# Performance work log

Hardware: AMD Instinct MI355X
Metric: run time of the kernel (lower is better)

The kernel has to match this reference:

```python
import jax, jax.numpy as jnp
import numpy as np

N_ENT = 50000
N_REL = 500
N_EDGE = 800000
H_DIM = 96
BN_EPS = 1e-5


def setup_inputs() -> dict:
    key = jax.random.key(0)
    k1, k2, k3, k4, k5 = jax.random.split(key, 5)
    return {
        "ent_emb": jax.random.normal(k1, (N_ENT, H_DIM), dtype=jnp.float32),
        "rel_emb": jax.random.normal(k2, (N_REL, H_DIM), dtype=jnp.float32),
        "neigh_w": jax.random.normal(k3, (H_DIM, H_DIM), dtype=jnp.float32) * (1.0 / np.sqrt(H_DIM)),
        "bn_gamma": jnp.ones((H_DIM,), dtype=jnp.float32),
        "bn_beta": jnp.zeros((H_DIM,), dtype=jnp.float32),
        "rel_id": jax.random.randint(k4, (N_EDGE,), 0, N_REL, dtype=jnp.int64),
        "dst": jax.random.randint(k5, (N_EDGE,), 0, N_ENT, dtype=jnp.int64),
    }


def reference(ent_emb, rel_emb, neigh_w, bn_gamma, bn_beta, rel_id, dst):
    n_nodes = ent_emb.shape[0]
    # per-edge gather: edge feature = relation embedding  [E, D]
    e = rel_emb[rel_id]
    # e_dot_v: dot of edge feature with destination node embedding  [E]
    score = jnp.sum(e * ent_emb[dst], axis=-1)
    # edge softmax over incoming edges of each destination node
    seg_max = jax.ops.segment_max(score, dst, num_segments=n_nodes)  # [N]
    w = jnp.exp(score - seg_max[dst])                                # [E]
    seg_sum = jax.ops.segment_sum(w, dst, num_segments=n_nodes)      # [N]
    alpha = w / seg_sum[dst]                                         # [E]
    # weighted scatter-sum aggregation into destination nodes  [N, D]
    neigh = jax.ops.segment_sum(e * alpha[:, None], dst, num_segments=n_nodes)
    # linear
    out = neigh @ neigh_w
    # BatchNorm1d (training mode: batch stats over nodes, biased var)
    mu = jnp.mean(out, axis=0)
    var = jnp.mean((out - mu) ** 2, axis=0)
    out = (out - mu) * jax.lax.rsqrt(var + BN_EPS) * bn_gamma + bn_beta
    return jnp.tanh(out)
```

## Files before the change

kernel.cpp:

```cpp
#include <hip/hip_runtime.h>
#include <math.h>

#define N_ENT   50000
#define N_REL   500
#define N_EDGE  800000
#define H       96
#define BN_EPS  1e-5f
#define DEG_CAP 64

#define RELW_BLOCKS ((N_REL * H + 255) / 256)
#define ZERO_N      (N_ENT + 2 * H)
#define ZERO_BLOCKS ((ZERO_N + 255) / 256)

__global__ __launch_bounds__(256) void k_init(
        const float* __restrict__ rel, const float* __restrict__ W,
        float* __restrict__ relW, unsigned* __restrict__ zbase) {
    if (blockIdx.x < RELW_BLOCKS) {
        __shared__ float Ws[H * H];
        for (int i = threadIdx.x; i < H * H; i += 256) Ws[i] = W[i];
        __syncthreads();
        int t = blockIdx.x * 256 + threadIdx.x;
        if (t >= N_REL * H) return;
        int r = t / H;
        int c = t - r * H;
        const float4* rr = (const float4*)(rel + (size_t)r * H);
        float acc = 0.0f;
#pragma unroll
        for (int i = 0; i < H / 4; ++i) {
            float4 a = rr[i];
            acc += a.x * Ws[(4 * i + 0) * H + c];
            acc += a.y * Ws[(4 * i + 1) * H + c];
            acc += a.z * Ws[(4 * i + 2) * H + c];
            acc += a.w * Ws[(4 * i + 3) * H + c];
        }
        relW[t] = acc;
    } else {
        int i = (blockIdx.x - RELW_BLOCKS) * 256 + threadIdx.x;
        if (i < ZERO_N) zbase[i] = 0u;
    }
}

__global__ __launch_bounds__(256) void k_bucket(
        const int* __restrict__ dst, const int* __restrict__ rel_id,
        int* __restrict__ cursor, unsigned short* __restrict__ pay) {
    int e = blockIdx.x * 256 + threadIdx.x;
    if (e >= N_EDGE) return;
    int d = dst[e];
    int r = rel_id[e];
    int p = atomicAdd(cursor + d, 1);
    if (p < DEG_CAP) pay[d * DEG_CAP + p] = (unsigned short)r;
}

__global__ __launch_bounds__(256) void k_node(
        const float* __restrict__ ent, const float* __restrict__ rel,
        const unsigned short* __restrict__ pay, const int* __restrict__ cursor,
        const float* __restrict__ relW, float* __restrict__ out) {
    __shared__ float sh_w[4][DEG_CAP];
    __shared__ int   sh_r[4][DEG_CAP];
    int wv   = threadIdx.x >> 6;
    int lane = threadIdx.x & 63;
    int n = blockIdx.x * 4 + wv;
    if (n >= N_ENT) return;
    int cnt = min(cursor[n], DEG_CAP);

    {
        int q  = lane & 3;
        int jj = lane >> 2;
        const float4* er = (const float4*)(ent + (size_t)n * H) + q * 6;
        float4 e0 = er[0], e1 = er[1], e2 = er[2], e3 = er[3], e4 = er[4], e5 = er[5];
        int npass = (cnt + 15) >> 4;
        for (int p = 0; p < npass; ++p) {
            int j = (p << 4) + jj;
            bool valid = (j < cnt);
            int rid = valid ? (int)pay[n * DEG_CAP + j] : 0;
            float part = 0.0f;
            if (valid) {
                const float4* rr = (const float4*)(rel + (size_t)rid * H) + q * 6;
                float4 b;
                b = rr[0]; part += e0.x*b.x + e0.y*b.y + e0.z*b.z + e0.w*b.w;
                b = rr[1]; part += e1.x*b.x + e1.y*b.y + e1.z*b.z + e1.w*b.w;
                b = rr[2]; part += e2.x*b.x + e2.y*b.y + e2.z*b.z + e2.w*b.w;
                b = rr[3]; part += e3.x*b.x + e3.y*b.y + e3.z*b.z + e3.w*b.w;
                b = rr[4]; part += e4.x*b.x + e4.y*b.y + e4.z*b.z + e4.w*b.w;
                b = rr[5]; part += e5.x*b.x + e5.y*b.y + e5.z*b.z + e5.w*b.w;
            }
            part += __shfl_xor(part, 1);
            part += __shfl_xor(part, 2);
            if (valid && q == 0) { sh_w[wv][j] = part; sh_r[wv][j] = rid; }
        }
    }

    {
        float sc = (lane < cnt) ? sh_w[wv][lane] : -INFINITY;
        float m = sc;
#pragma unroll
        for (int off = 1; off < 64; off <<= 1)
            m = fmaxf(m, __shfl_xor(m, off));
        float w = (lane < cnt) ? __expf(sc - m) : 0.0f;
        float s = w;
#pragma unroll
        for (int off = 1; off < 64; off <<= 1)
            s += __shfl_xor(s, off);
        float inv = (cnt > 0) ? 1.0f / s : 0.0f;
        if (lane < cnt) sh_w[wv][lane] = w * inv;
    }

    int g  = lane & 7;
    int es = lane >> 3;
    float4 a0 = make_float4(0.f, 0.f, 0.f, 0.f);
    float4 a1 = make_float4(0.f, 0.f, 0.f, 0.f);
    float4 a2 = make_float4(0.f, 0.f, 0.f, 0.f);
    for (int k = es; k < cnt; k += 8) {
        float w  = sh_w[wv][k];
        int rid  = sh_r[wv][k];
        const float4* p = (const float4*)(relW + (size_t)rid * H + g * 12);
        float4 f0 = p[0], f1 = p[1], f2 = p[2];
        a0.x += w * f0.x; a0.y += w * f0.y; a0.z += w * f0.z; a0.w += w * f0.w;
        a1.x += w * f1.x; a1.y += w * f1.y; a1.z += w * f1.z; a1.w += w * f1.w;
        a2.x += w * f2.x; a2.y += w * f2.y; a2.z += w * f2.z; a2.w += w * f2.w;
    }
#pragma unroll
    for (int off = 8; off < 64; off <<= 1) {
        a0.x += __shfl_xor(a0.x, off); a0.y += __shfl_xor(a0.y, off);
        a0.z += __shfl_xor(a0.z, off); a0.w += __shfl_xor(a0.w, off);
        a1.x += __shfl_xor(a1.x, off); a1.y += __shfl_xor(a1.y, off);
        a1.z += __shfl_xor(a1.z, off); a1.w += __shfl_xor(a1.w, off);
        a2.x += __shfl_xor(a2.x, off); a2.y += __shfl_xor(a2.y, off);
        a2.z += __shfl_xor(a2.z, off); a2.w += __shfl_xor(a2.w, off);
    }
    if (es == 0) {
        float4* op = (float4*)(out + (size_t)n * H + g * 12);
        op[0] = a0; op[1] = a1; op[2] = a2;
    }
}

__global__ __launch_bounds__(256) void k_bnstats(
        const float* __restrict__ out, float* __restrict__ bn_sum,
        float* __restrict__ bn_sumsq) {
    __shared__ float sh_s[4][H], sh_q[4][H];
    int wave = threadIdx.x >> 6;
    int lane = threadIdx.x & 63;
    float4 s = make_float4(0.f, 0.f, 0.f, 0.f);
    float4 ss = make_float4(0.f, 0.f, 0.f, 0.f);
    if (lane < H / 4) {
        for (int n = blockIdx.x * 4 + wave; n < N_ENT; n += gridDim.x * 4) {
            float4 v = ((const float4*)(out + (size_t)n * H))[lane];
            s.x += v.x; s.y += v.y; s.z += v.z; s.w += v.w;
            ss.x += v.x * v.x; ss.y += v.y * v.y;
            ss.z += v.z * v.z; ss.w += v.w * v.w;
        }
        ((float4*)sh_s[wave])[lane] = s;
        ((float4*)sh_q[wave])[lane] = ss;
    }
    __syncthreads();
    int d = threadIdx.x;
    if (d < H) {
        float ts = sh_s[0][d] + sh_s[1][d] + sh_s[2][d] + sh_s[3][d];
        float tq = sh_q[0][d] + sh_q[1][d] + sh_q[2][d] + sh_q[3][d];
        atomicAdd(bn_sum + d, ts);
        atomicAdd(bn_sumsq + d, tq);
    }
}

__device__ __forceinline__ float fast_tanh(float x) {
    return 1.0f - 2.0f / (__expf(2.0f * x) + 1.0f);
}

__global__ __launch_bounds__(256) void k_bnapply(
        float* __restrict__ out, const float* __restrict__ bn_sum,
        const float* __restrict__ bn_sumsq, const float* __restrict__ gamma,
        const float* __restrict__ beta) {
    int t = blockIdx.x * 256 + threadIdx.x;
    if (t >= N_ENT * H / 4) return;
    int c4 = t % (H / 4);
    const float inv_n = 1.0f / (float)N_ENT;
    float4 v = ((const float4*)out)[t];
    float4 sm = ((const float4*)bn_sum)[c4];
    float4 sq = ((const float4*)bn_sumsq)[c4];
    float4 g  = ((const float4*)gamma)[c4];
    float4 b  = ((const float4*)beta)[c4];
    float mu0 = sm.x * inv_n, mu1 = sm.y * inv_n, mu2 = sm.z * inv_n, mu3 = sm.w * inv_n;
    float r0 = rsqrtf(sq.x * inv_n - mu0 * mu0 + BN_EPS);
    float r1 = rsqrtf(sq.y * inv_n - mu1 * mu1 + BN_EPS);
    float r2 = rsqrtf(sq.z * inv_n - mu2 * mu2 + BN_EPS);
    float r3 = rsqrtf(sq.w * inv_n - mu3 * mu3 + BN_EPS);
    float4 o;
    o.x = fast_tanh((v.x - mu0) * r0 * g.x + b.x);
    o.y = fast_tanh((v.y - mu1) * r1 * g.y + b.y);
    o.z = fast_tanh((v.z - mu2) * r2 * g.z + b.z);
    o.w = fast_tanh((v.w - mu3) * r3 * g.w + b.w);
    ((float4*)out)[t] = o;
}

extern "C" void kernel_launch(void* const* d_in, const int* in_sizes, int n_in,
                              void* d_out, int out_size, void* d_ws, size_t ws_size,
                              hipStream_t stream) {
    const float* ent   = (const float*)d_in[0];
    const float* rel   = (const float*)d_in[1];
    const float* W     = (const float*)d_in[2];
    const float* gamma = (const float*)d_in[3];
    const float* beta  = (const float*)d_in[4];
    const int* rel_id  = (const int*)d_in[5];
    const int* dst     = (const int*)d_in[6];
    float* out = (float*)d_out;

    float* ws       = (float*)d_ws;
    int*   cursor   = (int*)ws;
    float* bn_sum   = ws + N_ENT;
    float* bn_sumsq = bn_sum + H;
    float* relW     = bn_sumsq + H;
    unsigned short* pay = (unsigned short*)(relW + N_REL * H);

    k_init<<<RELW_BLOCKS + ZERO_BLOCKS, 256, 0, stream>>>(
        rel, W, relW, (unsigned*)cursor);
    k_bucket<<<(N_EDGE + 255) / 256, 256, 0, stream>>>(dst, rel_id, cursor, pay);
    k_node<<<(N_ENT + 3) / 4, 256, 0, stream>>>(ent, rel, pay, cursor, relW, out);
    k_bnstats<<<784, 256, 0, stream>>>(out, bn_sum, bn_sumsq);
    k_bnapply<<<(N_ENT * H / 4 + 255) / 256, 256, 0, stream>>>(
        out, bn_sum, bn_sumsq, gamma, beta);
}
```

Baseline: 205.7 us.

## Fuse BatchNorm statistics into node aggregation kernel with persistent grid

Folds the per-feature sum and sum-of-squares accumulation into the node aggregation kernel. The kernel now runs as a grid-stride persistent loop over a fixed number of blocks, so each wave keeps running partial sums in registers and reduces them through shared memory with one atomic per feature per block. This removes a separate launch and a full re-read of the 50000x96 intermediate output. In exchange, the node kernel carries more registers, which may lower occupancy, and its fixed block count may cause load imbalance.

Result: slower. 229.6 us (+11.6%).

```diff
diff --git a/kernel.cpp b/kernel.cpp
--- a/kernel.cpp
+++ b/kernel.cpp
@@ -11,6 +11,7 @@
 #define RELW_BLOCKS ((N_REL * H + 255) / 256)
 #define ZERO_N      (N_ENT + 2 * H)
 #define ZERO_BLOCKS ((ZERO_N + 255) / 256)
+#define NODE_BLOCKS 1568
 
 __global__ __launch_bounds__(256) void k_init(
         const float* __restrict__ rel, const float* __restrict__ W,
@@ -54,109 +55,108 @@
 __global__ __launch_bounds__(256) void k_node(
         const float* __restrict__ ent, const float* __restrict__ rel,
         const unsigned short* __restrict__ pay, const int* __restrict__ cursor,
-        const float* __restrict__ relW, float* __restrict__ out) {
+        const float* __restrict__ relW, float* __restrict__ out,
+        float* __restrict__ bn_sum, float* __restrict__ bn_sumsq) {
     __shared__ float sh_w[4][DEG_CAP];
     __shared__ int   sh_r[4][DEG_CAP];
+    __shared__ float sh_bs[4][H], sh_bq[4][H];
     int wv   = threadIdx.x >> 6;
     int lane = threadIdx.x & 63;
-    int n = blockIdx.x * 4 + wv;
-    if (n >= N_ENT) return;
-    int cnt = min(cursor[n], DEG_CAP);
-
-    {
-        int q  = lane & 3;
-        int jj = lane >> 2;
-        const float4* er = (const float4*)(ent + (size_t)n * H) + q * 6;
-        float4 e0 = er[0], e1 = er[1], e2 = er[2], e3 = er[3], e4 = er[4], e5 = er[5];
-        int npass = (cnt + 15) >> 4;
-        for (int p = 0; p < npass; ++p) {
-            int j = (p << 4) + jj;
-            bool valid = (j < cnt);
-            int rid = valid ? (int)pay[n * DEG_CAP + j] : 0;
-            float part = 0.0f;
-            if (valid) {
-                const float4* rr = (const float4*)(rel + (size_t)rid * H) + q * 6;
-                float4 b;
-                b = rr[0]; part += e0.x*b.x + e0.y*b.y + e0.z*b.z + e0.w*b.w;
-                b = rr[1]; part += e1.x*b.x + e1.y*b.y + e1.z*b.z + e1.w*b.w;
-                b = rr[2]; part += e2.x*b.x + e2.y*b.y + e2.z*b.z + e2.w*b.w;
-                b = rr[3]; part += e3.x*b.x + e3.y*b.y + e3.z*b.z + e3.w*b.w;
-                b = rr[4]; part += e4.x*b.x + e4.y*b.y + e4.z*b.z + e4.w*b.w;
-                b = rr[5]; part += e5.x*b.x + e5.y*b.y + e5.z*b.z + e5.w*b.w;
-            }
-            part += __shfl_xor(part, 1);
-            part += __shfl_xor(part, 2);
-            if (valid && q == 0) { sh_w[wv][j] = part; sh_r[wv][j] = rid; }
-        }
-    }
-
-    {
-        float sc = (lane < cnt) ? sh_w[wv][lane] : -INFINITY;
-        float m = sc;
-#pragma unroll
-        for (int off = 1; off < 64; off <<= 1)
-            m = fmaxf(m, __shfl_xor(m, off));
-        float w = (lane < cnt) ? __expf(sc - m) : 0.0f;
-        float s = w;
-#pragma unroll
-        for (int off = 1; off < 64; off <<= 1)
-            s += __shfl_xor(s, off);
-        float inv = (cnt > 0) ? 1.0f / s : 0.0f;
-        if (lane < cnt) sh_w[wv][lane] = w * inv;
-    }
-
+    int q  = lane & 3;
+    int jj = lane >> 2;
     int g  = lane & 7;
     int es = lane >> 3;
-    float4 a0 = make_float4(0.f, 0.f, 0.f, 0.f);
-    float4 a1 = make_float4(0.f, 0.f, 0.f, 0.f);
-    float4 a2 = make_float4(0.f, 0.f, 0.f, 0.f);
-    for (int k = es; k < cnt; k += 8) {
-        float w  = sh_w[wv][k];
-        int rid  = sh_r[wv][k];
-        const float4* p = (const float4*)(relW + (size_t)rid * H + g * 12);
-        float4 f0 = p[0], f1 = p[1], f2 = p[2];
-        a0.x += w * f0.x; a0.y += w * f0.y; a0.z += w * f0.z; a0.w += w * f0.w;
-        a1.x += w * f1.x; a1.y += w * f1.y; a1.z += w * f1.z; a1.w += w * f1.w;
-        a2.x += w * f2.x; a2.y += w * f2.y; a2.z += w * f2.z; a2.w += w * f2.w;
-    }
-#pragma unroll
-    for (int off = 8; off < 64; off <<= 1) {
-        a0.x += __shfl_xor(a0.x, off); a0.y += __shfl_xor(a0.y, off);
-        a0.z += __shfl_xor(a0.z, off); a0.w += __shfl_xor(a0.w, off);
-        a1.x += __shfl_xor(a1.x, off); a1.y += __shfl_xor(a1.y, off);
-        a1.z += __shfl_xor(a1.z, off); a1.w += __shfl_xor(a1.w, off);
-        a2.x += __shfl_xor(a2.x, off); a2.y += __shfl_xor(a2.y, off);
-        a2.z += __shfl_xor(a2.z, off); a2.w += __shfl_xor(a2.w, off);
-    }
+
+    float4 bs0 = make_float4(0.f,0.f,0.f,0.f), bs1 = bs0, bs2 = bs0;
+    float4 bq0 = bs0, bq1 = bs0, bq2 = bs0;
+
+    for (int n = blockIdx.x * 4 + wv; n < N_ENT; n += NODE_BLOCKS * 4) {
+        int cnt = min(cursor[n], DEG_CAP);
+
+        {
+            const float4* er = (const float4*)(ent + (size_t)n * H) + q * 6;
+            float4 e0 = er[0], e1 = er[1], e2 = er[2],
+                   e3 = er[3], e4 = er[4], e5 = er[5];
+            int npass = (cnt + 15) >> 4;
+            for (int p = 0; p < npass; ++p) {
+                int j = (p << 4) + jj;
+                bool valid = (j < cnt);
+                int rid = valid ? (int)pay[n * DEG_CAP + j] : 0;
+                float part = 0.0f;
+                if (valid) {
+                    const float4* rr = (const float4*)(rel + (size_t)rid * H) + q * 6;
+                    float4 b;
+                    b = rr[0]; part += e0.x*b.x + e0.y*b.y + e0.z*b.z + e0.w*b.w;
+                    b = rr[1]; part += e1.x*b.x + e1.y*b.y + e1.z*b.z + e1.w*b.w;
+                    b = rr[2]; part += e2.x*b.x + e2.y*b.y + e2.z*b.z + e2.w*b.w;
+                    b = rr[3]; part += e3.x*b.x + e3.y*b.y + e3.z*b.z + e3.w*b.w;
+                    b = rr[4]; part += e4.x*b.x + e4.y*b.y + e4.z*b.z + e4.w*b.w;
+                    b = rr[5]; part += e5.x*b.x + e5.y*b.y + e5.z*b.z + e5.w*b.w;
+                }
+                part += __shfl_xor(part, 1);
+                part += __shfl_xor(part, 2);
+                if (valid && q == 0) { sh_w[wv][j] = part; sh_r[wv][j] = rid; }
+            }
+        }
+
+        {
+            float sc = (lane < cnt) ? sh_w[wv][lane] : -INFINITY;
+            float m = sc;
+#pragma unroll
+            for (int off = 1; off < 64; off <<= 1)
+                m = fmaxf(m, __shfl_xor(m, off));
+            float w = (lane < cnt) ? __expf(sc - m) : 0.0f;
+            float s = w;
+#pragma unroll
+            for (int off = 1; off < 64; off <<= 1)
+                s += __shfl_xor(s, off);
+            float inv = (cnt > 0) ? 1.0f / s : 0.0f;
+            if (lane < cnt) sh_w[wv][lane] = w * inv;
+        }
+
+        float4 a0 = make_float4(0.f,0.f,0.f,0.f);
+        float4 a1 = a0, a2 = a0;
+        for (int k = es; k < cnt; k += 8) {
+            float w  = sh_w[wv][k];
+            int rid  = sh_r[wv][k];
+            const float4* p = (const float4*)(relW + (size_t)rid * H + g * 12);
+            float4 f0 = p[0], f1 = p[1], f2 = p[2];
+            a0.x += w * f0.x; a0.y += w * f0.y; a0.z += w * f0.z; a0.w += w * f0.w;
+            a1.x += w * f1.x; a1.y += w * f1.y; a1.z += w * f1.z; a1.w += w * f1.w;
+            a2.x += w * f2.x; a2.y += w * f2.y; a2.z += w * f2.z; a2.w += w * f2.w;
+        }
+#pragma unroll
+        for (int off = 8; off < 64; off <<= 1) {
+            a0.x += __shfl_xor(a0.x, off); a0.y += __shfl_xor(a0.y, off);
+            a0.z += __shfl_xor(a0.z, off); a0.w += __shfl_xor(a0.w, off);
+            a1.x += __shfl_xor(a1.x, off); a1.y += __shfl_xor(a1.y, off);
+            a1.z += __shfl_xor(a1.z, off); a1.w += __shfl_xor(a1.w, off);
+            a2.x += __shfl_xor(a2.x, off); a2.y += __shfl_xor(a2.y, off);
+            a2.z += __shfl_xor(a2.z, off); a2.w += __shfl_xor(a2.w, off);
+        }
+        if (es == 0) {
+            float4* op = (float4*)(out + (size_t)n * H + g * 12);
+            op[0] = a0; op[1] = a1; op[2] = a2;
+            bs0.x += a0.x; bs0.y += a0.y; bs0.z += a0.z; bs0.w += a0.w;
+            bs1.x += a1.x; bs1.y += a1.y; bs1.z += a1.z; bs1.w += a1.w;
+            bs2.x += a2.x; bs2.y += a2.y; bs2.z += a2.z; bs2.w += a2.w;
+            bq0.x += a0.x*a0.x; bq0.y += a0.y*a0.y; bq0.z += a0.z*a0.z; bq0.w += a0.w*a0.w;
+            bq1.x += a1.x*a1.x; bq1.y += a1.y*a1.y; bq1.z += a1.z*a1.z; bq1.w += a1.w*a1.w;
+            bq2.x += a2.x*a2.x; bq2.y += a2.y*a2.y; bq2.z += a2.z*a2.z; bq2.w += a2.w*a2.w;
+        }
+    }
+
     if (es == 0) {
-        float4* op = (float4*)(out + (size_t)n * H + g * 12);
-        op[0] = a0; op[1] = a1; op[2] = a2;
-    }
-}
-
-__global__ __launch_bounds__(256) void k_bnstats(
-        const float* __restrict__ out, float* __restrict__ bn_sum,
-        float* __restrict__ bn_sumsq) {
-    __shared__ float sh_s[4][H], sh_q[4][H];
-    int wave = threadIdx.x >> 6;
-    int lane = threadIdx.x & 63;
-    float4 s = make_float4(0.f, 0.f, 0.f, 0.f);
-    float4 ss = make_float4(0.f, 0.f, 0.f, 0.f);
-    if (lane < H / 4) {
-        for (int n = blockIdx.x * 4 + wave; n < N_ENT; n += gridDim.x * 4) {
-            float4 v = ((const float4*)(out + (size_t)n * H))[lane];
-            s.x += v.x; s.y += v.y; s.z += v.z; s.w += v.w;
-            ss.x += v.x * v.x; ss.y += v.y * v.y;
-            ss.z += v.z * v.z; ss.w += v.w * v.w;
-        }
-        ((float4*)sh_s[wave])[lane] = s;
-        ((float4*)sh_q[wave])[lane] = ss;
+        float4* ps = (float4*)(sh_bs[wv] + g * 12);
+        float4* pq = (float4*)(sh_bq[wv] + g * 12);
+        ps[0] = bs0; ps[1] = bs1; ps[2] = bs2;
+        pq[0] = bq0; pq[1] = bq1; pq[2] = bq2;
     }
     __syncthreads();
     int d = threadIdx.x;
     if (d < H) {
-        float ts = sh_s[0][d] + sh_s[1][d] + sh_s[2][d] + sh_s[3][d];
-        float tq = sh_q[0][d] + sh_q[1][d] + sh_q[2][d] + sh_q[3][d];
+        float ts = sh_bs[0][d] + sh_bs[1][d] + sh_bs[2][d] + sh_bs[3][d];
+        float tq = sh_bq[0][d] + sh_bq[1][d] + sh_bq[2][d] + sh_bq[3][d];
         atomicAdd(bn_sum + d, ts);
         atomicAdd(bn_sumsq + d, tq);
     }
@@ -214,8 +214,8 @@
     k_init<<<RELW_BLOCKS + ZERO_BLOCKS, 256, 0, stream>>>(
         rel, W, relW, (unsigned*)cursor);
     k_bucket<<<(N_EDGE + 255) / 256, 256, 0, stream>>>(dst, rel_id, cursor, pay);
-    k_node<<<(N_ENT + 3) / 4, 256, 0, stream>>>(ent, rel, pay, cursor, relW, out);
-    k_bnstats<<<784, 256, 0, stream>>>(out, bn_sum, bn_sumsq);
+    k_node<<<NODE_BLOCKS, 256, 0, stream>>>(
+        ent, rel, pay, cursor, relW, out, bn_sum, bn_sumsq);
     k_bnapply<<<(N_ENT * H / 4 + 255) / 256, 256, 0, stream>>>(
         out, bn_sum, bn_sumsq, gamma, beta);
 }
```
